# Optimization experiments

Measured on AMD Instinct MI355X. Metric: run time of the kernel, lower is better.

## Reference

```python
import jax, jax.numpy as jnp
import numpy as np

B, T, C, H = 8, 4096, 1024, 64

def setup_inputs() -> dict:
    key = jax.random.key(0)
    k1, k2, k3, k4 = jax.random.split(key, 4)
    return {
        "x": jax.random.normal(k1, (B, T, C), dtype=jnp.float32),
        "Wq": jax.random.normal(k2, (C, H), dtype=jnp.float32) * (C ** -0.5),
        "Wk": jax.random.normal(k3, (C, H), dtype=jnp.float32) * (C ** -0.5),
        "Wv": jax.random.normal(k4, (C, H), dtype=jnp.float32) * (C ** -0.5),
    }

def reference(x, Wq, Wk, Wv):
    # x: [B, T, C]; projections are bias-free Linears
    q = jnp.einsum("btc,ch->bth", x, Wq)  # [B, T, H]
    k = jnp.einsum("btc,ch->bth", x, Wk)
    v = jnp.einsum("btc,ch->bth", x, Wv)
    # NOTE: original scales by C**-0.5 (embed size), not head_size**-0.5
    scores = jnp.einsum("bqh,bkh->bqk", q, k) * (x.shape[-1] ** -0.5)  # [B, T, T]
    causal = jnp.tril(jnp.ones((x.shape[1], x.shape[1]), dtype=bool))
    scores = jnp.where(causal, scores, -jnp.inf)
    weights = jax.nn.softmax(scores, axis=-1)
    # dropout p=0.0 (eval) -> identity
    return jnp.einsum("bqk,bkh->bqh", weights, v)  # [B, T, H]
```

## Files before the change

kernel.cpp:

```cpp
#include <hip/hip_runtime.h>
#include <hip/hip_bf16.h>

typedef __attribute__((ext_vector_type(8))) short short8;
typedef __attribute__((ext_vector_type(4))) float f32x4;
typedef unsigned short u16;
typedef unsigned int u32;
typedef unsigned long long u64;

typedef u64    __attribute__((may_alias)) u64a;
typedef short8 __attribute__((may_alias)) short8a;
typedef float4 __attribute__((may_alias)) float4a;

#define Tseq 4096
#define LPP  72

__device__ __forceinline__ u32 pk_bf(float a, float b) {
    union { __hip_bfloat162 h; u32 u; } t;
    float2 f; f.x = a; f.y = b;
    t.h = __float22bfloat162_rn(f);
    return t.u;
}

__device__ __forceinline__ u16 f2bf(float f) {
    u32 u = __float_as_uint(f);
    u = (u + 0x7FFFu + ((u >> 16) & 1u)) >> 16;
    return (u16)u;
}

__device__ __forceinline__ short8 ld_frag_lds(const u16* p) {
    union { short8 v; u64 u[2]; } t;
    t.u[0] = *(const u64a*)(p);
    t.u[1] = *(const u64a*)(p + 4);
    return t.v;
}

__device__ __forceinline__ short8 cvt8(float4 a, float4 b) {
    union { short8 s; u32 u[4]; } t;
    t.u[0] = pk_bf(a.x, a.y); t.u[1] = pk_bf(a.z, a.w);
    t.u[2] = pk_bf(b.x, b.y); t.u[3] = pk_bf(b.z, b.w);
    return t.s;
}

__device__ __forceinline__ void gld_lds16(const void* g, void* l) {
    __builtin_amdgcn_global_load_lds(
        (const __attribute__((address_space(1))) u32*)g,
        (__attribute__((address_space(3))) u32*)l, 16, 0, 0);
}

__global__ __launch_bounds__(256) void wt_kernel(const float* __restrict__ Wq,
                                                 const float* __restrict__ Wk,
                                                 const float* __restrict__ Wv,
                                                 u16* __restrict__ wtf) {
    int idx = blockIdx.x * 256 + threadIdx.x;
    int lane = idx & 63, cc = (idx >> 6) & 31, n = (idx >> 11) & 3, mat = idx >> 13;
    const float* W = (mat == 0) ? Wq : ((mat == 1) ? Wk : Wv);
    float sc = (mat == 0) ? 0.03125f : 1.0f;
    int h = n * 16 + (lane & 15);
    int cbase = cc * 32 + (lane >> 4) * 8;
    union { short8 s; u32 u[4]; } t;
#pragma unroll
    for (int j2 = 0; j2 < 4; ++j2) {
        float a = W[(size_t)(cbase + j2 * 2)     * 64 + h] * sc;
        float b = W[(size_t)(cbase + j2 * 2 + 1) * 64 + h] * sc;
        t.u[j2] = pk_bf(a, b);
    }
    *(short8a*)(wtf + (size_t)idx * 8) = t.s;
}

__global__ __launch_bounds__(256, 2) void proj_kernel(const float* __restrict__ x,
                                                      const u16* __restrict__ wtf,
                                                      u16* __restrict__ qb,
                                                      u16* __restrict__ kA,
                                                      u16* __restrict__ vA) {
    __shared__ __align__(16) u16 Wl[2][12 * 2 * 64 * 8];

    const int tid = threadIdx.x, lane = tid & 63, wave = tid >> 6;
    const int m = lane & 15, quad = lane >> 4;
    const long rowbase = (long)blockIdx.x * 64 + wave * 16;
    const float* xr = x + (rowbase + m) * 1024 + quad * 8;

    f32x4 acc[12];
#pragma unroll
    for (int i = 0; i < 12; ++i) acc[i] = (f32x4){0.f, 0.f, 0.f, 0.f};

#define STAGE(p, buf)                                                          \
    {                                                                          \
        _Pragma("unroll")                                                      \
        for (int i = 0; i < 6; ++i) {                                          \
            int c = wave * 6 + i, mn = c >> 1, ccp = c & 1;                    \
            const u16* g = wtf + ((size_t)(mn * 32 + (p) * 2 + ccp) * 64 + lane) * 8; \
            u16* l = &Wl[buf][(size_t)(mn * 2 + ccp) * 512];                   \
            gld_lds16(g, l);                                                   \
        }                                                                      \
    }

    float4 xa[4], xb[4];
#pragma unroll
    for (int t = 0; t < 4; ++t)
        xa[t] = *(const float4a*)(xr + (t >> 1) * 32 + (t & 1) * 4);
#pragma unroll
    for (int t = 0; t < 4; ++t)
        xb[t] = *(const float4a*)(xr + (2 + (t >> 1)) * 32 + (t & 1) * 4);

    STAGE(0, 0);
    __syncthreads();

    for (int p = 0; p < 16; ++p) {
        if (p < 15) STAGE(p + 1, (p + 1) & 1);
        float4 xn[4];
        if (p < 14) {
#pragma unroll
            for (int t = 0; t < 4; ++t)
                xn[t] = *(const float4a*)(xr + (2 * (p + 2) + (t >> 1)) * 32 + (t & 1) * 4);
        }
        const u16* wb = Wl[p & 1];
#pragma unroll
        for (int ccp = 0; ccp < 2; ++ccp) {
            short8 af = cvt8(xa[ccp * 2], xa[ccp * 2 + 1]);
#pragma unroll
            for (int mn = 0; mn < 12; ++mn) {
                short8 bf = *(const short8a*)(wb + ((size_t)(mn * 2 + ccp) * 64 + lane) * 8);
                acc[mn] = __builtin_amdgcn_mfma_f32_16x16x32_bf16(af, bf, acc[mn], 0, 0, 0);
            }
        }
#pragma unroll
        for (int t = 0; t < 4; ++t) { xa[t] = xb[t]; if (p < 14) xb[t] = xn[t]; }
        __syncthreads();
    }
#undef STAGE

    const int b  = (int)(rowbase >> 12);
    const int tb = (int)(rowbase & 4095);

#pragma unroll
    for (int n = 0; n < 4; ++n)
#pragma unroll
        for (int r = 0; r < 4; ++r)
            qb[(rowbase + quad * 4 + r) * 64 + n * 16 + m] = f2bf(acc[n][r]);

#pragma unroll
    for (int n = 0; n < 4; ++n) {
        int kk = n >> 1;
        int lq = (n * 2 + (m >> 3)) & 3;
        int j  = m & 7;
#pragma unroll
        for (int r = 0; r < 4; ++r) {
            int key = tb + quad * 4 + r;
            size_t a = ((((size_t)b * 256 + (key >> 4)) * 2 + kk) * 64
                        + ((key & 15) + 16 * lq)) * 8 + j;
            kA[a] = f2bf(acc[4 + n][r]);
        }
    }

    {
        int key0 = tb + quad * 4;
        int j0 = key0 & 7;
        int q2 = (key0 >> 3) & 3;
        int kc = key0 >> 5;
#pragma unroll
        for (int n = 0; n < 4; ++n) {
            u64 pv = (u64)pk_bf(acc[8 + n][0], acc[8 + n][1])
                   | ((u64)pk_bf(acc[8 + n][2], acc[8 + n][3]) << 32);
            size_t a = ((((size_t)b * 4 + n) * 128 + kc) * 64 + (m + 16 * q2)) * 8 + j0;
            *(u64a*)(vA + a) = pv;
        }
    }
}

struct K8 { short8 k[8]; };

__device__ __forceinline__ void loadK(K8& f, const u16* kAb, int kt, int lane) {
    const u16* kp = kAb + (size_t)kt * 4096 + (size_t)lane * 8;
#pragma unroll
    for (int mt = 0; mt < 4; ++mt) {
        f.k[mt * 2]     = *(const short8a*)(kp + mt * 1024);
        f.k[mt * 2 + 1] = *(const short8a*)(kp + mt * 1024 + 512);
    }
}

__device__ __forceinline__ void attn_step(const K8& f, const u16* vAb,
        short8 qf0, short8 qf1, u16* pw,
        f32x4& o0, f32x4& o1, f32x4& o2, f32x4& o3,
        float& lsum, int kt, int n_s, int qrow, int quad, int m, int lane) {
    const float L2E = 1.4426950408889634f;
    const float FMB = 4.0f * L2E;
    const u16* vp = vAb + (size_t)kt * 1024 + (size_t)lane * 8;
    short8 vf[8];
#pragma unroll
    for (int ht = 0; ht < 4; ++ht) {
        vf[ht * 2]     = *(const short8a*)(vp + (size_t)ht * 65536);
        vf[ht * 2 + 1] = *(const short8a*)(vp + (size_t)ht * 65536 + 512);
    }
    f32x4 s[4];
#pragma unroll
    for (int mt = 0; mt < 4; ++mt) {
        f32x4 a = (f32x4){0.f, 0.f, 0.f, 0.f};
        a = __builtin_amdgcn_mfma_f32_16x16x32_bf16(f.k[mt * 2],     qf0, a, 0, 0, 0);
        a = __builtin_amdgcn_mfma_f32_16x16x32_bf16(f.k[mt * 2 + 1], qf1, a, 0, 0, 0);
        s[mt] = a;
    }
    if (kt == n_s) {
#pragma unroll
        for (int mt = 0; mt < 4; ++mt)
#pragma unroll
            for (int r = 0; r < 4; ++r) {
                int key = kt * 64 + mt * 16 + quad * 4 + r;
                if (key > qrow) s[mt][r] = -1e30f;
            }
    }
#pragma unroll
    for (int mt = 0; mt < 4; ++mt) {
        float p0 = __builtin_amdgcn_exp2f(s[mt][0] * L2E - FMB);
        float p1 = __builtin_amdgcn_exp2f(s[mt][1] * L2E - FMB);
        float p2 = __builtin_amdgcn_exp2f(s[mt][2] * L2E - FMB);
        float p3 = __builtin_amdgcn_exp2f(s[mt][3] * L2E - FMB);
        lsum += (p0 + p1) + (p2 + p3);
        u64 pv = (u64)pk_bf(p0, p1) | ((u64)pk_bf(p2, p3) << 32);
        *(u64a*)(pw + m * LPP + mt * 16 + quad * 4) = pv;
    }
    __builtin_amdgcn_wave_barrier();
    short8 pf0 = ld_frag_lds(pw + m * LPP + quad * 8);
    short8 pf1 = ld_frag_lds(pw + m * LPP + 32 + quad * 8);
    o0 = __builtin_amdgcn_mfma_f32_16x16x32_bf16(vf[0], pf0, o0, 0, 0, 0);
    o0 = __builtin_amdgcn_mfma_f32_16x16x32_bf16(vf[1], pf1, o0, 0, 0, 0);
    o1 = __builtin_amdgcn_mfma_f32_16x16x32_bf16(vf[2], pf0, o1, 0, 0, 0);
    o1 = __builtin_amdgcn_mfma_f32_16x16x32_bf16(vf[3], pf1, o1, 0, 0, 0);
    o2 = __builtin_amdgcn_mfma_f32_16x16x32_bf16(vf[4], pf0, o2, 0, 0, 0);
    o2 = __builtin_amdgcn_mfma_f32_16x16x32_bf16(vf[5], pf1, o2, 0, 0, 0);
    o3 = __builtin_amdgcn_mfma_f32_16x16x32_bf16(vf[6], pf0, o3, 0, 0, 0);
    o3 = __builtin_amdgcn_mfma_f32_16x16x32_bf16(vf[7], pf1, o3, 0, 0, 0);
}

__global__ __launch_bounds__(256, 3) void attn_kernel(const u16* __restrict__ qb,
                                                      const u16* __restrict__ kA,
                                                      const u16* __restrict__ vA,
                                                      float* __restrict__ out) {
    __shared__ __align__(16) u16 Pt[4][16 * LPP];
    __shared__ float Ob[4][16][64];
    __shared__ float Lb[4][64];

    const int tid = threadIdx.x, lane = tid & 63, wave = tid >> 6;
    const int m = lane & 15, quad = lane >> 4;
    const int beta = blockIdx.x;
    const int b = beta & 7, u = beta >> 3;

    const int T0 = (u >> 2) + 1;
    const int T1 = 64 - (u >> 2);
    const int max13 = (T0 > (T1 + 2) / 3) ? T0 : (T1 + 2) / 3;
    const int c22a = (T0 + 1) >> 1, c22b = (T1 + 1) >> 1;
    const int max22 = (c22a > c22b) ? c22a : c22b;
    const int n0 = (max13 <= max22) ? 1 : 2;
    const int n1 = 4 - n0;

    const int r = (wave + beta) & 3;
    const int strip_id = (r < n0) ? 0 : 1;
    const int part   = strip_id ? (r - n0) : r;
    const int nparts = strip_id ? n1 : n0;
    const int T      = strip_id ? T1 : T0;
    const int s      = strip_id ? (255 - u) : u;
    const int qbase = s * 16;
    const int n_s = s >> 2;
    const int kt0 = part * T / nparts;
    const int kt1 = (part + 1) * T / nparts - 1;

    const u16* qp = qb + ((size_t)b * Tseq + qbase + m) * 64;
    short8 qf0 = *(const short8a*)(qp + quad * 8);
    short8 qf1 = *(const short8a*)(qp + 32 + quad * 8);

    const u16* kAb = kA + (size_t)b * (256 * 2 * 64 * 8);
    const u16* vAb = vA + (size_t)b * (4 * 128 * 64 * 8);
    u16* pw = Pt[wave];

    f32x4 o0 = {0.f, 0.f, 0.f, 0.f}, o1 = o0, o2 = o0, o3 = o0;
    float lsum = 0.f;
    const int qrow = qbase + m;

    if (kt0 <= kt1) {
        K8 ka, kb2;
        loadK(ka, kAb, kt0, lane);
        int kt = kt0;
        while (true) {
            if (kt < kt1) loadK(kb2, kAb, kt + 1, lane);
            attn_step(ka, vAb, qf0, qf1, pw, o0, o1, o2, o3, lsum,
                      kt, n_s, qrow, quad, m, lane);
            if (kt == kt1) break;
            ++kt;
            if (kt < kt1) loadK(ka, kAb, kt + 1, lane);
            attn_step(kb2, vAb, qf0, qf1, pw, o0, o1, o2, o3, lsum,
                      kt, n_s, qrow, quad, m, lane);
            if (kt == kt1) break;
            ++kt;
        }
    }

    if (part != 0) {
        Ob[r][0][lane] = o0[0]; Ob[r][1][lane] = o0[1];
        Ob[r][2][lane] = o0[2]; Ob[r][3][lane] = o0[3];
        Ob[r][4][lane] = o1[0]; Ob[r][5][lane] = o1[1];
        Ob[r][6][lane] = o1[2]; Ob[r][7][lane] = o1[3];
        Ob[r][8][lane] = o2[0]; Ob[r][9][lane] = o2[1];
        Ob[r][10][lane] = o2[2]; Ob[r][11][lane] = o2[3];
        Ob[r][12][lane] = o3[0]; Ob[r][13][lane] = o3[1];
        Ob[r][14][lane] = o3[2]; Ob[r][15][lane] = o3[3];
        Lb[r][lane] = lsum;
    }
    __syncthreads();
    if (part == 0) {
#pragma unroll 1
        for (int pr = 1; pr < nparts; ++pr) {
            const int rr = r + pr;
            o0[0] += Ob[rr][0][lane]; o0[1] += Ob[rr][1][lane];
            o0[2] += Ob[rr][2][lane]; o0[3] += Ob[rr][3][lane];
            o1[0] += Ob[rr][4][lane]; o1[1] += Ob[rr][5][lane];
            o1[2] += Ob[rr][6][lane]; o1[3] += Ob[rr][7][lane];
            o2[0] += Ob[rr][8][lane]; o2[1] += Ob[rr][9][lane];
            o2[2] += Ob[rr][10][lane]; o2[3] += Ob[rr][11][lane];
            o3[0] += Ob[rr][12][lane]; o3[1] += Ob[rr][13][lane];
            o3[2] += Ob[rr][14][lane]; o3[3] += Ob[rr][15][lane];
            lsum += Lb[rr][lane];
        }

        lsum += __shfl_xor(lsum, 16, 64);
        lsum += __shfl_xor(lsum, 32, 64);
        float inv = 1.0f / lsum;

        float* orow = out + ((size_t)b * Tseq + qbase + m) * 64;
        float4 w;
        w.x = o0[0] * inv; w.y = o0[1] * inv; w.z = o0[2] * inv; w.w = o0[3] * inv;
        *(float4a*)(orow + 0 * 16 + quad * 4) = w;
        w.x = o1[0] * inv; w.y = o1[1] * inv; w.z = o1[2] * inv; w.w = o1[3] * inv;
        *(float4a*)(orow + 1 * 16 + quad * 4) = w;
        w.x = o2[0] * inv; w.y = o2[1] * inv; w.z = o2[2] * inv; w.w = o2[3] * inv;
        *(float4a*)(orow + 2 * 16 + quad * 4) = w;
        w.x = o3[0] * inv; w.y = o3[1] * inv; w.z = o3[2] * inv; w.w = o3[3] * inv;
        *(float4a*)(orow + 3 * 16 + quad * 4) = w;
    }
}

extern "C" void kernel_launch(void* const* d_in, const int* in_sizes, int n_in,
                              void* d_out, int out_size, void* d_ws, size_t ws_size,
                              hipStream_t stream) {
    const float* x  = (const float*)d_in[0];
    const float* Wq = (const float*)d_in[1];
    const float* Wk = (const float*)d_in[2];
    const float* Wv = (const float*)d_in[3];
    float* out = (float*)d_out;

    char* ws = (char*)d_ws;
    u16* wtf = (u16*)ws;
    u16* qb  = (u16*)(ws + 512 * 1024);
    u16* kA  = (u16*)(ws + 512 * 1024 + 4 * 1024 * 1024);
    u16* vA  = (u16*)(ws + 512 * 1024 + 8 * 1024 * 1024);

    wt_kernel<<<96, 256, 0, stream>>>(Wq, Wk, Wv, wtf);
    proj_kernel<<<512, 256, 0, stream>>>(x, wtf, qb, kA, vA);
    attn_kernel<<<1024, 256, 0, stream>>>(qb, kA, vA, out);
}
```

Baseline: 252.3 us.

## Process two 16-row query tiles per wave to reuse K/V fragments

Each wave now handles 32 query rows (two 16-row sub-tiles) per strip, so every loaded K and V fragment feeds two score/PV computations. This halves global K/V traffic per query row, and the grid shrinks from 1024 to 512 blocks with launch bounds lowered to 2 blocks per CU. It also wraps MFMA sections in s_setprio raises. The costs are higher register and LDS pressure, lower occupancy, and coarser causal load balancing across fewer blocks.

```diff
diff --git a/kernel.cpp b/kernel.cpp
--- a/kernel.cpp
+++ b/kernel.cpp
@@ -178,20 +178,23 @@
     }
 }
 
-__device__ __forceinline__ void attn_step(const K8& f, const u16* vAb,
-        short8 qf0, short8 qf1, u16* pw,
-        f32x4& o0, f32x4& o1, f32x4& o2, f32x4& o3,
-        float& lsum, int kt, int n_s, int qrow, int quad, int m, int lane) {
-    const float L2E = 1.4426950408889634f;
-    const float FMB = 4.0f * L2E;
+__device__ __forceinline__ void loadV(short8* vf, const u16* vAb, int kt, int lane) {
     const u16* vp = vAb + (size_t)kt * 1024 + (size_t)lane * 8;
-    short8 vf[8];
 #pragma unroll
     for (int ht = 0; ht < 4; ++ht) {
         vf[ht * 2]     = *(const short8a*)(vp + (size_t)ht * 65536);
         vf[ht * 2 + 1] = *(const short8a*)(vp + (size_t)ht * 65536 + 512);
     }
+}
+
+__device__ __forceinline__ void sub_step(const K8& f, const short8* vf,
+        short8 qf0, short8 qf1, u16* pw,
+        f32x4& o0, f32x4& o1, f32x4& o2, f32x4& o3,
+        float& lsum, int kt, int n_s, int qrow, int quad, int m) {
+    const float L2E = 1.4426950408889634f;
+    const float FMB = 4.0f * L2E;
     f32x4 s[4];
+    __builtin_amdgcn_s_setprio(1);
 #pragma unroll
     for (int mt = 0; mt < 4; ++mt) {
         f32x4 a = (f32x4){0.f, 0.f, 0.f, 0.f};
@@ -199,6 +202,7 @@
         a = __builtin_amdgcn_mfma_f32_16x16x32_bf16(f.k[mt * 2 + 1], qf1, a, 0, 0, 0);
         s[mt] = a;
     }
+    __builtin_amdgcn_s_setprio(0);
     if (kt == n_s) {
 #pragma unroll
         for (int mt = 0; mt < 4; ++mt)
@@ -221,6 +225,7 @@
     __builtin_amdgcn_wave_barrier();
     short8 pf0 = ld_frag_lds(pw + m * LPP + quad * 8);
     short8 pf1 = ld_frag_lds(pw + m * LPP + 32 + quad * 8);
+    __builtin_amdgcn_s_setprio(1);
     o0 = __builtin_amdgcn_mfma_f32_16x16x32_bf16(vf[0], pf0, o0, 0, 0, 0);
     o0 = __builtin_amdgcn_mfma_f32_16x16x32_bf16(vf[1], pf1, o0, 0, 0, 0);
     o1 = __builtin_amdgcn_mfma_f32_16x16x32_bf16(vf[2], pf0, o1, 0, 0, 0);
@@ -229,23 +234,24 @@
     o2 = __builtin_amdgcn_mfma_f32_16x16x32_bf16(vf[5], pf1, o2, 0, 0, 0);
     o3 = __builtin_amdgcn_mfma_f32_16x16x32_bf16(vf[6], pf0, o3, 0, 0, 0);
     o3 = __builtin_amdgcn_mfma_f32_16x16x32_bf16(vf[7], pf1, o3, 0, 0, 0);
-}
-
-__global__ __launch_bounds__(256, 3) void attn_kernel(const u16* __restrict__ qb,
+    __builtin_amdgcn_s_setprio(0);
+}
+
+__global__ __launch_bounds__(256, 2) void attn_kernel(const u16* __restrict__ qb,
                                                       const u16* __restrict__ kA,
                                                       const u16* __restrict__ vA,
                                                       float* __restrict__ out) {
-    __shared__ __align__(16) u16 Pt[4][16 * LPP];
-    __shared__ float Ob[4][16][64];
-    __shared__ float Lb[4][64];
+    __shared__ __align__(16) u16 Pt[4][2][16 * LPP];
+    __shared__ float Ob[4][2][16][64];
+    __shared__ float Lb[4][2][64];
 
     const int tid = threadIdx.x, lane = tid & 63, wave = tid >> 6;
     const int m = lane & 15, quad = lane >> 4;
     const int beta = blockIdx.x;
     const int b = beta & 7, u = beta >> 3;
 
-    const int T0 = (u >> 2) + 1;
-    const int T1 = 64 - (u >> 2);
+    const int T0 = (u >> 1) + 1;
+    const int T1 = 64 - (u >> 1);
     const int max13 = (T0 > (T1 + 2) / 3) ? T0 : (T1 + 2) / 3;
     const int c22a = (T0 + 1) >> 1, c22b = (T1 + 1) >> 1;
     const int max22 = (c22a > c22b) ? c22a : c22b;
@@ -257,83 +263,126 @@
     const int part   = strip_id ? (r - n0) : r;
     const int nparts = strip_id ? n1 : n0;
     const int T      = strip_id ? T1 : T0;
-    const int s      = strip_id ? (255 - u) : u;
-    const int qbase = s * 16;
-    const int n_s = s >> 2;
+    const int s32    = strip_id ? (127 - u) : u;
+    const int qbase = s32 * 32;
+    const int n_s = s32 >> 1;
     const int kt0 = part * T / nparts;
     const int kt1 = (part + 1) * T / nparts - 1;
 
-    const u16* qp = qb + ((size_t)b * Tseq + qbase + m) * 64;
-    short8 qf0 = *(const short8a*)(qp + quad * 8);
-    short8 qf1 = *(const short8a*)(qp + 32 + quad * 8);
+    const u16* qpA = qb + ((size_t)b * Tseq + qbase + m) * 64;
+    const u16* qpB = qpA + 16 * 64;
+    short8 qA0 = *(const short8a*)(qpA + quad * 8);
+    short8 qA1 = *(const short8a*)(qpA + 32 + quad * 8);
+    short8 qB0 = *(const short8a*)(qpB + quad * 8);
+    short8 qB1 = *(const short8a*)(qpB + 32 + quad * 8);
 
     const u16* kAb = kA + (size_t)b * (256 * 2 * 64 * 8);
     const u16* vAb = vA + (size_t)b * (4 * 128 * 64 * 8);
-    u16* pw = Pt[wave];
-
-    f32x4 o0 = {0.f, 0.f, 0.f, 0.f}, o1 = o0, o2 = o0, o3 = o0;
-    float lsum = 0.f;
-    const int qrow = qbase + m;
+    u16* pwA = Pt[wave][0];
+    u16* pwB = Pt[wave][1];
+
+    f32x4 oA0 = {0.f, 0.f, 0.f, 0.f}, oA1 = oA0, oA2 = oA0, oA3 = oA0;
+    f32x4 oB0 = oA0, oB1 = oA0, oB2 = oA0, oB3 = oA0;
+    float lsumA = 0.f, lsumB = 0.f;
+    const int qrowA = qbase + m;
+    const int qrowB = qbase + 16 + m;
 
     if (kt0 <= kt1) {
         K8 ka, kb2;
+        short8 vf[8];
         loadK(ka, kAb, kt0, lane);
         int kt = kt0;
         while (true) {
+            loadV(vf, vAb, kt, lane);
             if (kt < kt1) loadK(kb2, kAb, kt + 1, lane);
-            attn_step(ka, vAb, qf0, qf1, pw, o0, o1, o2, o3, lsum,
-                      kt, n_s, qrow, quad, m, lane);
+            sub_step(ka, vf, qA0, qA1, pwA, oA0, oA1, oA2, oA3, lsumA,
+                     kt, n_s, qrowA, quad, m);
+            sub_step(ka, vf, qB0, qB1, pwB, oB0, oB1, oB2, oB3, lsumB,
+                     kt, n_s, qrowB, quad, m);
             if (kt == kt1) break;
             ++kt;
+            loadV(vf, vAb, kt, lane);
             if (kt < kt1) loadK(ka, kAb, kt + 1, lane);
-            attn_step(kb2, vAb, qf0, qf1, pw, o0, o1, o2, o3, lsum,
-                      kt, n_s, qrow, quad, m, lane);
+            sub_step(kb2, vf, qA0, qA1, pwA, oA0, oA1, oA2, oA3, lsumA,
+                     kt, n_s, qrowA, quad, m);
+            sub_step(kb2, vf, qB0, qB1, pwB, oB0, oB1, oB2, oB3, lsumB,
+                     kt, n_s, qrowB, quad, m);
             if (kt == kt1) break;
             ++kt;
         }
     }
 
     if (part != 0) {
-        Ob[r][0][lane] = o0[0]; Ob[r][1][lane] = o0[1];
-        Ob[r][2][lane] = o0[2]; Ob[r][3][lane] = o0[3];
-        Ob[r][4][lane] = o1[0]; Ob[r][5][lane] = o1[1];
-        Ob[r][6][lane] = o1[2]; Ob[r][7][lane] = o1[3];
-        Ob[r][8][lane] = o2[0]; Ob[r][9][lane] = o2[1];
-        Ob[r][10][lane] = o2[2]; Ob[r][11][lane] = o2[3];
-        Ob[r][12][lane] = o3[0]; Ob[r][13][lane] = o3[1];
-        Ob[r][14][lane] = o3[2]; Ob[r][15][lane] = o3[3];
-        Lb[r][lane] = lsum;
+        Ob[r][0][0][lane] = oA0[0]; Ob[r][0][1][lane] = oA0[1];
+        Ob[r][0][2][lane] = oA0[2]; Ob[r][0][3][lane] = oA0[3];
+        Ob[r][0][4][lane] = oA1[0]; Ob[r][0][5][lane] = oA1[1];
+        Ob[r][0][6][lane] = oA1[2]; Ob[r][0][7][lane] = oA1[3];
+        Ob[r][0][8][lane] = oA2[0]; Ob[r][0][9][lane] = oA2[1];
+        Ob[r][0][10][lane] = oA2[2]; Ob[r][0][11][lane] = oA2[3];
+        Ob[r][0][12][lane] = oA3[0]; Ob[r][0][13][lane] = oA3[1];
+        Ob[r][0][14][lane] = oA3[2]; Ob[r][0][15][lane] = oA3[3];
+        Lb[r][0][lane] = lsumA;
+        Ob[r][1][0][lane] = oB0[0]; Ob[r][1][1][lane] = oB0[1];
+        Ob[r][1][2][lane] = oB0[2]; Ob[r][1][3][lane] = oB0[3];
+        Ob[r][1][4][lane] = oB1[0]; Ob[r][1][5][lane] = oB1[1];
+        Ob[r][1][6][lane] = oB1[2]; Ob[r][1][7][lane] = oB1[3];
+        Ob[r][1][8][lane] = oB2[0]; Ob[r][1][9][lane] = oB2[1];
+        Ob[r][1][10][lane] = oB2[2]; Ob[r][1][11][lane] = oB2[3];
+        Ob[r][1][12][lane] = oB3[0]; Ob[r][1][13][lane] = oB3[1];
+        Ob[r][1][14][lane] = oB3[2]; Ob[r][1][15][lane] = oB3[3];
+        Lb[r][1][lane] = lsumB;
     }
     __syncthreads();
     if (part == 0) {
 #pragma unroll 1
         for (int pr = 1; pr < nparts; ++pr) {
             const int rr = r + pr;
-            o0[0] += Ob[rr][0][lane]; o0[1] += Ob[rr][1][lane];
-            o0[2] += Ob[rr][2][lane]; o0[3] += Ob[rr][3][lane];
-            o1[0] += Ob[rr][4][lane]; o1[1] += Ob[rr][5][lane];
-            o1[2] += Ob[rr][6][lane]; o1[3] += Ob[rr][7][lane];
-            o2[0] += Ob[rr][8][lane]; o2[1] += Ob[rr][9][lane];
-            o2[2] += Ob[rr][10][lane]; o2[3] += Ob[rr][11][lane];
-            o3[0] += Ob[rr][12][lane]; o3[1] += Ob[rr][13][lane];
-            o3[2] += Ob[rr][14][lane]; o3[3] += Ob[rr][15][lane];
-            lsum += Lb[rr][lane];
-        }
-
-        lsum += __shfl_xor(lsum, 16, 64);
-        lsum += __shfl_xor(lsum, 32, 64);
-        float inv = 1.0f / lsum;
-
-        float* orow = out + ((size_t)b * Tseq + qbase + m) * 64;
+            oA0[0] += Ob[rr][0][0][lane]; oA0[1] += Ob[rr][0][1][lane];
+            oA0[2] += Ob[rr][0][2][lane]; oA0[3] += Ob[rr][0][3][lane];
+            oA1[0] += Ob[rr][0][4][lane]; oA1[1] += Ob[rr][0][5][lane];
+            oA1[2] += Ob[rr][0][6][lane]; oA1[3] += Ob[rr][0][7][lane];
+            oA2[0] += Ob[rr][0][8][lane]; oA2[1] += Ob[rr][0][9][lane];
+            oA2[2] += Ob[rr][0][10][lane]; oA2[3] += Ob[rr][0][11][lane];
+            oA3[0] += Ob[rr][0][12][lane]; oA3[1] += Ob[rr][0][13][lane];
+            oA3[2] += Ob[rr][0][14][lane]; oA3[3] += Ob[rr][0][15][lane];
+            lsumA += Lb[rr][0][lane];
+            oB0[0] += Ob[rr][1][0][lane]; oB0[1] += Ob[rr][1][1][lane];
+            oB0[2] += Ob[rr][1][2][lane]; oB0[3] += Ob[rr][1][3][lane];
+            oB1[0] += Ob[rr][1][4][lane]; oB1[1] += Ob[rr][1][5][lane];
+            oB1[2] += Ob[rr][1][6][lane]; oB1[3] += Ob[rr][1][7][lane];
+            oB2[0] += Ob[rr][1][8][lane]; oB2[1] += Ob[rr][1][9][lane];
+            oB2[2] += Ob[rr][1][10][lane]; oB2[3] += Ob[rr][1][11][lane];
+            oB3[0] += Ob[rr][1][12][lane]; oB3[1] += Ob[rr][1][13][lane];
+            oB3[2] += Ob[rr][1][14][lane]; oB3[3] += Ob[rr][1][15][lane];
+            lsumB += Lb[rr][1][lane];
+        }
+
+        lsumA += __shfl_xor(lsumA, 16, 64);
+        lsumA += __shfl_xor(lsumA, 32, 64);
+        lsumB += __shfl_xor(lsumB, 16, 64);
+        lsumB += __shfl_xor(lsumB, 32, 64);
+        float invA = 1.0f / lsumA;
+        float invB = 1.0f / lsumB;
+
+        float* orowA = out + ((size_t)b * Tseq + qbase + m) * 64;
+        float* orowB = orowA + 16 * 64;
         float4 w;
-        w.x = o0[0] * inv; w.y = o0[1] * inv; w.z = o0[2] * inv; w.w = o0[3] * inv;
-        *(float4a*)(orow + 0 * 16 + quad * 4) = w;
-        w.x = o1[0] * inv; w.y = o1[1] * inv; w.z = o1[2] * inv; w.w = o1[3] * inv;
-        *(float4a*)(orow + 1 * 16 + quad * 4) = w;
-        w.x = o2[0] * inv; w.y = o2[1] * inv; w.z = o2[2] * inv; w.w = o2[3] * inv;
-        *(float4a*)(orow + 2 * 16 + quad * 4) = w;
-        w.x = o3[0] * inv; w.y = o3[1] * inv; w.z = o3[2] * inv; w.w = o3[3] * inv;
-        *(float4a*)(orow + 3 * 16 + quad * 4) = w;
+        w.x = oA0[0] * invA; w.y = oA0[1] * invA; w.z = oA0[2] * invA; w.w = oA0[3] * invA;
+        *(float4a*)(orowA + 0 * 16 + quad * 4) = w;
+        w.x = oA1[0] * invA; w.y = oA1[1] * invA; w.z = oA1[2] * invA; w.w = oA1[3] * invA;
+        *(float4a*)(orowA + 1 * 16 + quad * 4) = w;
+        w.x = oA2[0] * invA; w.y = oA2[1] * invA; w.z = oA2[2] * invA; w.w = oA2[3] * invA;
+        *(float4a*)(orowA + 2 * 16 + quad * 4) = w;
+        w.x = oA3[0] * invA; w.y = oA3[1] * invA; w.z = oA3[2] * invA; w.w = oA3[3] * invA;
+        *(float4a*)(orowA + 3 * 16 + quad * 4) = w;
+        w.x = oB0[0] * invB; w.y = oB0[1] * invB; w.z = oB0[2] * invB; w.w = oB0[3] * invB;
+        *(float4a*)(orowB + 0 * 16 + quad * 4) = w;
+        w.x = oB1[0] * invB; w.y = oB1[1] * invB; w.z = oB1[2] * invB; w.w = oB1[3] * invB;
+        *(float4a*)(orowB + 1 * 16 + quad * 4) = w;
+        w.x = oB2[0] * invB; w.y = oB2[1] * invB; w.z = oB2[2] * invB; w.w = oB2[3] * invB;
+        *(float4a*)(orowB + 2 * 16 + quad * 4) = w;
+        w.x = oB3[0] * invB; w.y = oB3[1] * invB; w.z = oB3[2] * invB; w.w = oB3[3] * invB;
+        *(float4a*)(orowB + 3 * 16 + quad * 4) = w;
     }
 }
 
@@ -354,5 +403,5 @@
 
     wt_kernel<<<96, 256, 0, stream>>>(Wq, Wk, Wv, wtf);
     proj_kernel<<<512, 256, 0, stream>>>(x, wtf, qb, kA, vA);
-    attn_kernel<<<1024, 256, 0, stream>>>(qb, kA, vA, out);
-}
+    attn_kernel<<<512, 256, 0, stream>>>(qb, kA, vA, out);
+}
```

Result: faster. 239.8 us (-4.9%).
